# Kernel optimization log

Measured on AMD Instinct MI355X. Metric: run time of the kernel, lower is better.

Reference implementation:

```python
import jax, jax.numpy as jnp
import numpy as np

B, T, F = 8192, 336, 8
H = 20        # lstm_hidden_size
DENSE = 20
OUT = 1
N_LAYERS = 3


def _param(key, shape, scale):
    return jax.random.uniform(key, shape, jnp.float32, -scale, scale)


def setup_inputs() -> dict:
    key = jax.random.key(0)
    ks = jax.random.split(key, 32)
    s = 1.0 / np.sqrt(H)
    inp = {"x": jax.random.normal(ks[0], (B, T, F), jnp.float32)}
    k = 1
    for l in range(N_LAYERS):
        in_size = F if l == 0 else H
        inp[f"W_ih{l}"] = _param(ks[k], (4 * H, in_size), s); k += 1
        inp[f"W_hh{l}"] = _param(ks[k], (4 * H, H), s); k += 1
        inp[f"b_ih{l}"] = _param(ks[k], (4 * H,), s); k += 1
        inp[f"b_hh{l}"] = _param(ks[k], (4 * H,), s); k += 1
    inp["fc1_w"] = _param(ks[k], (DENSE, H), 1.0 / np.sqrt(H)); k += 1
    inp["fc1_b"] = _param(ks[k], (DENSE,), 1.0 / np.sqrt(H)); k += 1
    inp["fc2_w"] = _param(ks[k], (OUT, DENSE), 1.0 / np.sqrt(DENSE)); k += 1
    inp["fc2_b"] = _param(ks[k], (OUT,), 1.0 / np.sqrt(DENSE)); k += 1
    return inp


def lstm_layer(x, W_ih, W_hh, b_ih, b_hh):
    """PyTorch-convention LSTM over [B, T, in]; returns hidden sequence [B, T, H]."""
    b = x.shape[0]
    # Precompute input contribution for all timesteps in one GEMM: [B, T, 4H]
    xg = jnp.einsum('bti,gi->btg', x, W_ih) + b_ih + b_hh
    W_hh_T = W_hh.T  # [H, 4H]

    def step(carry, xt):
        h, c = carry
        gates = xt + h @ W_hh_T                      # [B, 4H], gate order i,f,g,o
        i, f, g, o = jnp.split(gates, 4, axis=-1)
        i = jax.nn.sigmoid(i)
        f = jax.nn.sigmoid(f)
        g = jnp.tanh(g)
        o = jax.nn.sigmoid(o)
        c = f * c + i * g
        h = o * jnp.tanh(c)
        return (h, c), h

    h0 = jnp.zeros((b, W_hh.shape[1]), x.dtype)
    c0 = jnp.zeros_like(h0)
    _, hs = jax.lax.scan(step, (h0, c0), jnp.swapaxes(xg, 0, 1))  # [T, B, H]
    return jnp.swapaxes(hs, 0, 1)


def reference(x, W_ih0, W_hh0, b_ih0, b_hh0, W_ih1, W_hh1, b_ih1, b_hh1,
              W_ih2, W_hh2, b_ih2, b_hh2, fc1_w, fc1_b, fc2_w, fc2_b):
    layers = [(W_ih0, W_hh0, b_ih0, b_hh0),
              (W_ih1, W_hh1, b_ih1, b_hh1),
              (W_ih2, W_hh2, b_ih2, b_hh2)]
    h = x
    for (wi, wh, bi, bh) in layers:
        h = lstm_layer(h, wi, wh, bi, bh)
    h = h[:, -1, :]                         # last timestep, [B, H]
    # dropout layers are identity at inference
    h = jax.nn.relu(h @ fc1_w.T + fc1_b)    # [B, DENSE]
    return h @ fc2_w.T + fc2_b              # [B, OUT]
```

## Files before the change

kernel.cpp:

```cpp
#include <hip/hip_runtime.h>


#define T_LEN 336

typedef _Float16 f16;
typedef _Float16 f16x2 __attribute__((ext_vector_type(2)));
typedef _Float16 f16x4 __attribute__((ext_vector_type(4)));
typedef _Float16 f16x8 __attribute__((ext_vector_type(8)));
typedef float f32x4 __attribute__((ext_vector_type(4)));

#define MFMA(a, b, c) __builtin_amdgcn_mfma_f32_16x16x32_f16((a), (b), (c), 0, 0, 0)

#define SWZ1(n, c) ((c) ^ (((n) & 7) << 3))
#define SWZ0(n, c) ((c) ^ (((n) & 3) << 3))

__device__ __forceinline__ float sigm(float x) {
  return __builtin_amdgcn_rcpf(1.0f + __builtin_amdgcn_exp2f(-1.4426950408889634f * x));
}
__device__ __forceinline__ float tanh_fast(float x) {
  return 2.0f * __builtin_amdgcn_rcpf(1.0f + __builtin_amdgcn_exp2f(-2.8853900817779268f * x)) - 1.0f;
}

#define CELLS4(DI, DF, DG, DO, HV) {                                                        \
  { float i_=sigm((DI)[0]), f_=sigm((DF)[0]), g_=tanh_fast((DG)[0]), o_=sigm((DO)[0]);      \
    c0 = f_*c0 + i_*g_; (HV)[0] = (f16)(o_*tanh_fast(c0)); }                                \
  { float i_=sigm((DI)[1]), f_=sigm((DF)[1]), g_=tanh_fast((DG)[1]), o_=sigm((DO)[1]);      \
    c1 = f_*c1 + i_*g_; (HV)[1] = (f16)(o_*tanh_fast(c1)); }                                \
  { float i_=sigm((DI)[2]), f_=sigm((DF)[2]), g_=tanh_fast((DG)[2]), o_=sigm((DO)[2]);      \
    c2 = f_*c2 + i_*g_; (HV)[2] = (f16)(o_*tanh_fast(c2)); }                                \
  { float i_=sigm((DI)[3]), f_=sigm((DF)[3]), g_=tanh_fast((DG)[3]), o_=sigm((DO)[3]);      \
    c3 = f_*c3 + i_*g_; (HV)[3] = (f16)(o_*tanh_fast(c3)); } }

#define CELL_L(DL, HOUT, GB) {                                                              \
  *(f32x4*)&GB[(q * 16 + n) * 4] = (DL);                                                    \
  float i_ = sigm(GB[n * 4 + q]);                                                           \
  float f_ = sigm(GB[(16 + n) * 4 + q]);                                                    \
  float g_ = tanh_fast(GB[(32 + n) * 4 + q]);                                               \
  float o_ = sigm(GB[(48 + n) * 4 + q]);                                                    \
  cL = f_*cL + i_*g_; HOUT = (f16)(o_*tanh_fast(cL)); }

__global__ __launch_bounds__(192, 2) void lstm3_ws_kernel(
    const float* __restrict__ x,
    const float* __restrict__ Wih0, const float* __restrict__ Whh0,
    const float* __restrict__ bih0, const float* __restrict__ bhh0,
    const float* __restrict__ Wih1, const float* __restrict__ Whh1,
    const float* __restrict__ bih1, const float* __restrict__ bhh1,
    const float* __restrict__ Wih2, const float* __restrict__ Whh2,
    const float* __restrict__ bih2, const float* __restrict__ bhh2,
    const float* __restrict__ fc1w, const float* __restrict__ fc1b,
    const float* __restrict__ fc2w, const float* __restrict__ fc2b,
    float* __restrict__ out)
{
  __shared__ __align__(16) f16 zT0[16 * 32];
  __shared__ __align__(16) f16 zT1[2][16 * 64];
  __shared__ __align__(16) f16 zT2[2][16 * 64];
  __shared__ __align__(16) float gbuf[3][256];
  __shared__ __align__(16) float pbuf[64];

  const int tid  = threadIdx.x;
  const int w    = tid >> 6;
  const int lane = tid & 63;
  const int n = lane & 15;
  const int q = lane >> 4;

  {
    f16x8 zer;
#pragma unroll
    for (int j = 0; j < 8; ++j) zer[j] = (f16)0.f;
    for (int i = tid; i < 64; i += 192)  ((f16x8*)zT0)[i] = zer;
    for (int i = tid; i < 256; i += 192) ((f16x8*)&zT1[0][0])[i] = zer;
    for (int i = tid; i < 256; i += 192) ((f16x8*)&zT2[0][0])[i] = zer;
  }
  __syncthreads();

  auto rowmap = [](int T, int m) { return T < 4 ? T * 20 + m : (m >> 2) * 20 + 16 + (m & 3); };

  f16x8 Fa0{}, Fa1{}, Fa2{}, Fa3{}, Fa4{};
  f16x8 Fb0{}, Fb1{}, Fb2{}, Fb3{}, Fb4{};
  f32x4 Bi{}, Bf{}, Bg{}, Bo{}, BL{};
  float c0 = 0.f, c1 = 0.f, c2 = 0.f, c3 = 0.f, cL = 0.f;

  if (w == 0) {
    auto gA0 = [&](int T) {
      int row = rowmap(T, n);
      f16x8 r;
#pragma unroll
      for (int j = 0; j < 8; ++j) {
        int k = q * 8 + j;
        float v = (k < 8) ? Wih0[row * 8 + k] : (k < 28 ? Whh0[row * 20 + k - 8] : 0.f);
        r[j] = (f16)v;
      }
      return r;
    };
    Fa0 = gA0(0); Fa1 = gA0(1); Fa2 = gA0(2); Fa3 = gA0(3); Fa4 = gA0(4);
    auto gB = [&](int T) {
      f32x4 r;
#pragma unroll
      for (int j = 0; j < 4; ++j) { int row = rowmap(T, q * 4 + j); r[j] = bih0[row] + bhh0[row]; }
      return r;
    };
    Bi = gB(0); Bf = gB(1); Bg = gB(2); Bo = gB(3); BL = gB(4);
  } else {
    const float* Wi = (w == 1) ? Wih1 : Wih2;
    const float* Wh = (w == 1) ? Whh1 : Whh2;
    const float* bi = (w == 1) ? bih1 : bih2;
    const float* bh = (w == 1) ? bhh1 : bhh2;
    auto gA = [&](int T, int c) {
      int row = rowmap(T, n);
      f16x8 r;
#pragma unroll
      for (int j = 0; j < 8; ++j) {
        int k = c * 32 + q * 8 + j;
        float v = (k < 20) ? Wi[row * 20 + k] : (k < 40 ? Wh[row * 20 + k - 20] : 0.f);
        r[j] = (f16)v;
      }
      return r;
    };
    Fa0 = gA(0, 0); Fb0 = gA(0, 1);
    Fa1 = gA(1, 0); Fb1 = gA(1, 1);
    Fa2 = gA(2, 0); Fb2 = gA(2, 1);
    Fa3 = gA(3, 0); Fb3 = gA(3, 1);
    Fa4 = gA(4, 0); Fb4 = gA(4, 1);
    auto gB = [&](int T) {
      f32x4 r;
#pragma unroll
      for (int j = 0; j < 4; ++j) { int row = rowmap(T, q * 4 + j); r[j] = bi[row] + bh[row]; }
      return r;
    };
    Bi = gB(0); Bf = gB(1); Bg = gB(2); Bo = gB(3); BL = gB(4);
  }

  const float* xb = x + (size_t)(blockIdx.x * 16 + n) * (T_LEN * 8) + 4 * q;
  f32x4 xA{}, xB{};
  if (w == 0) {
    xA = *(const f32x4*)(xb);
    xB = *(const f32x4*)(xb + 16);
  }

#pragma unroll 1
  for (int i = 0; i <= T_LEN + 1; ++i) {
    asm volatile("" ::: "memory");
    if (w == 0) {
      if (i < T_LEN) {
        if ((q >> 1) == (i & 1)) {
          f16x4 xh;
          xh[0] = (f16)xA[0]; xh[1] = (f16)xA[1]; xh[2] = (f16)xA[2]; xh[3] = (f16)xA[3];
          *(f16x4*)&zT0[n * 32 + SWZ0(n, 4 * (q & 1))] = xh;
        }
        if (i & 1) {
          xA = xB;
          int pn = (i >> 1) + 2;
          if (pn > (T_LEN / 2 - 1)) pn = T_LEN / 2 - 1;
          xB = *(const f32x4*)(xb + pn * 16);
        }
        f16x8 b0 = *(const f16x8*)&zT0[n * 32 + SWZ0(n, q * 8)];
        f32x4 di = MFMA(Fa0, b0, Bi), df = MFMA(Fa1, b0, Bf),
              dg = MFMA(Fa2, b0, Bg), dn = MFMA(Fa3, b0, Bo),
              dl = MFMA(Fa4, b0, BL);
        f16x4 hv; CELLS4(di, df, dg, dn, hv)
        f16* d1 = &zT1[i & 1][0];
        *(f16x4*)&zT0[n * 32 + SWZ0(n, 8 + q * 4)] = hv;
        *(f16x4*)&d1[n * 64 + SWZ1(n, q * 4)] = hv;
        f16 hl; CELL_L(dl, hl, gbuf[0])
        zT0[n * 32 + SWZ0(n, 24 + q)] = hl;
        d1[n * 64 + SWZ1(n, 16 + q)] = hl;
      }
    } else if (w == 1) {
      if (i >= 1 && i <= T_LEN) {
        const f16* src = &zT1[(i - 1) & 1][0];
        f16x8 ba = *(const f16x8*)&src[n * 64 + SWZ1(n, q * 8)];
        f16x8 bb = *(const f16x8*)&src[n * 64 + SWZ1(n, 32 + q * 8)];
        f32x4 di = MFMA(Fb0, bb, MFMA(Fa0, ba, Bi));
        f32x4 df = MFMA(Fb1, bb, MFMA(Fa1, ba, Bf));
        f32x4 dg = MFMA(Fb2, bb, MFMA(Fa2, ba, Bg));
        f32x4 dn = MFMA(Fb3, bb, MFMA(Fa3, ba, Bo));
        f32x4 dl = MFMA(Fb4, bb, MFMA(Fa4, ba, BL));
        f16x4 hv; CELLS4(di, df, dg, dn, hv)
        f16* d1 = &zT1[i & 1][0];
        f16* d2 = &zT2[i & 1][0];
        *(f16x4*)&d1[n * 64 + SWZ1(n, 20 + q * 4)] = hv;
        *(f16x4*)&d2[n * 64 + SWZ1(n, q * 4)] = hv;
        f16 hl; CELL_L(dl, hl, gbuf[1])
        d1[n * 64 + SWZ1(n, 36 + q)] = hl;
        d2[n * 64 + SWZ1(n, 16 + q)] = hl;
      }
    } else {
      if (i >= 2) {
        const f16* src = &zT2[(i - 1) & 1][0];
        f16x8 ba = *(const f16x8*)&src[n * 64 + SWZ1(n, q * 8)];
        f16x8 bb = *(const f16x8*)&src[n * 64 + SWZ1(n, 32 + q * 8)];
        f32x4 di = MFMA(Fb0, bb, MFMA(Fa0, ba, Bi));
        f32x4 df = MFMA(Fb1, bb, MFMA(Fa1, ba, Bf));
        f32x4 dg = MFMA(Fb2, bb, MFMA(Fa2, ba, Bg));
        f32x4 dn = MFMA(Fb3, bb, MFMA(Fa3, ba, Bo));
        f32x4 dl = MFMA(Fb4, bb, MFMA(Fa4, ba, BL));
        f16x4 hv; CELLS4(di, df, dg, dn, hv)
        f16* d2 = &zT2[i & 1][0];
        *(f16x4*)&d2[n * 64 + SWZ1(n, 20 + q * 4)] = hv;
        f16 hl; CELL_L(dl, hl, gbuf[2])
        d2[n * 64 + SWZ1(n, 36 + q)] = hl;
      }
    }
    asm volatile("s_waitcnt lgkmcnt(0)\n\ts_barrier" ::: "memory");
  }

  if (w == 2) {
    const f16* hb = &zT2[(T_LEN + 1) & 1][0];
    f16x4 hv0 = *(const f16x4*)&hb[n * 64 + SWZ1(n, 20)];
    f16x4 hv1 = *(const f16x4*)&hb[n * 64 + SWZ1(n, 24)];
    f16x4 hv2 = *(const f16x4*)&hb[n * 64 + SWZ1(n, 28)];
    f16x4 hv3 = *(const f16x4*)&hb[n * 64 + SWZ1(n, 32)];
    f16x4 hv4 = *(const f16x4*)&hb[n * 64 + SWZ1(n, 36)];
    float p = 0.f;
#pragma unroll
    for (int i = 0; i < 5; ++i) {
      int d = q * 5 + i;
      const float* wr = fc1w + d * 20;
      float s = fc1b[d]
        + wr[0]  * (float)hv0[0] + wr[1]  * (float)hv0[1] + wr[2]  * (float)hv0[2] + wr[3]  * (float)hv0[3]
        + wr[4]  * (float)hv1[0] + wr[5]  * (float)hv1[1] + wr[6]  * (float)hv1[2] + wr[7]  * (float)hv1[3]
        + wr[8]  * (float)hv2[0] + wr[9]  * (float)hv2[1] + wr[10] * (float)hv2[2] + wr[11] * (float)hv2[3]
        + wr[12] * (float)hv3[0] + wr[13] * (float)hv3[1] + wr[14] * (float)hv3[2] + wr[15] * (float)hv3[3]
        + wr[16] * (float)hv4[0] + wr[17] * (float)hv4[1] + wr[18] * (float)hv4[2] + wr[19] * (float)hv4[3];
      p += fc2w[d] * fmaxf(s, 0.f);
    }
    pbuf[n * 4 + q] = p;
    if (q == 0) {
      f32x4 pv = *(const f32x4*)&pbuf[n * 4];
      out[blockIdx.x * 16 + n] = pv[0] + pv[1] + pv[2] + pv[3] + fc2b[0];
    }
  }
}

extern "C" void kernel_launch(void* const* d_in, const int* in_sizes, int n_in,
                              void* d_out, int out_size, void* d_ws, size_t ws_size,
                              hipStream_t stream) {
  const float* x    = (const float*)d_in[0];
  const float* Wih0 = (const float*)d_in[1];
  const float* Whh0 = (const float*)d_in[2];
  const float* bih0 = (const float*)d_in[3];
  const float* bhh0 = (const float*)d_in[4];
  const float* Wih1 = (const float*)d_in[5];
  const float* Whh1 = (const float*)d_in[6];
  const float* bih1 = (const float*)d_in[7];
  const float* bhh1 = (const float*)d_in[8];
  const float* Wih2 = (const float*)d_in[9];
  const float* Whh2 = (const float*)d_in[10];
  const float* bih2 = (const float*)d_in[11];
  const float* bhh2 = (const float*)d_in[12];
  const float* fc1w = (const float*)d_in[13];
  const float* fc1b = (const float*)d_in[14];
  const float* fc2w = (const float*)d_in[15];
  const float* fc2b = (const float*)d_in[16];
  float* out = (float*)d_out;

  hipLaunchKernelGGL(lstm3_ws_kernel, dim3(8192 / 16), dim3(192), 0, stream,
                     x, Wih0, Whh0, bih0, bhh0,
                     Wih1, Whh1, bih1, bhh1,
                     Wih2, Whh2, bih2, bhh2,
                     fc1w, fc1b, fc2w, fc2b, out);
}
```

Baseline: 463.1 us.

## Process two timesteps per barrier and remap leftover gate rows to avoid LDS transpose

The wavefront-specialized pipeline now runs two LSTM timesteps per loop iteration, so each layer wave does two dependent cell updates between block barriers and the number of barriers is roughly halved. Each layer keeps its own hidden state in a separate ping-pong slot and publishes to the next layer's double-buffered slots. The leftover-gate rows are remapped so each lane holds all four gates of its hidden unit in registers, which removes the per-step gbuf LDS round trip. In exchange it uses more LDS buffers, longer serial chains per barrier interval and more complex index bookkeeping.

Result: faster. 415.2 us (-10.3%).

```diff
diff --git a/kernel.cpp b/kernel.cpp
--- a/kernel.cpp
+++ b/kernel.cpp
@@ -2,9 +2,9 @@
 
 
 #define T_LEN 336
+#define NJ 169
 
 typedef _Float16 f16;
-typedef _Float16 f16x2 __attribute__((ext_vector_type(2)));
 typedef _Float16 f16x4 __attribute__((ext_vector_type(4)));
 typedef _Float16 f16x8 __attribute__((ext_vector_type(8)));
 typedef float f32x4 __attribute__((ext_vector_type(4)));
@@ -12,7 +12,6 @@
 #define MFMA(a, b, c) __builtin_amdgcn_mfma_f32_16x16x32_f16((a), (b), (c), 0, 0, 0)
 
 #define SWZ1(n, c) ((c) ^ (((n) & 7) << 3))
-#define SWZ0(n, c) ((c) ^ (((n) & 3) << 3))
 
 __device__ __forceinline__ float sigm(float x) {
   return __builtin_amdgcn_rcpf(1.0f + __builtin_amdgcn_exp2f(-1.4426950408889634f * x));
@@ -21,7 +20,7 @@
   return 2.0f * __builtin_amdgcn_rcpf(1.0f + __builtin_amdgcn_exp2f(-2.8853900817779268f * x)) - 1.0f;
 }
 
-#define CELLS4(DI, DF, DG, DO, HV) {                                                        \
+#define CELLS5(DI, DF, DG, DO, DL, HV, HL) {                                                \
   { float i_=sigm((DI)[0]), f_=sigm((DF)[0]), g_=tanh_fast((DG)[0]), o_=sigm((DO)[0]);      \
     c0 = f_*c0 + i_*g_; (HV)[0] = (f16)(o_*tanh_fast(c0)); }                                \
   { float i_=sigm((DI)[1]), f_=sigm((DF)[1]), g_=tanh_fast((DG)[1]), o_=sigm((DO)[1]);      \
@@ -29,15 +28,39 @@
   { float i_=sigm((DI)[2]), f_=sigm((DF)[2]), g_=tanh_fast((DG)[2]), o_=sigm((DO)[2]);      \
     c2 = f_*c2 + i_*g_; (HV)[2] = (f16)(o_*tanh_fast(c2)); }                                \
   { float i_=sigm((DI)[3]), f_=sigm((DF)[3]), g_=tanh_fast((DG)[3]), o_=sigm((DO)[3]);      \
-    c3 = f_*c3 + i_*g_; (HV)[3] = (f16)(o_*tanh_fast(c3)); } }
-
-#define CELL_L(DL, HOUT, GB) {                                                              \
-  *(f32x4*)&GB[(q * 16 + n) * 4] = (DL);                                                    \
-  float i_ = sigm(GB[n * 4 + q]);                                                           \
-  float f_ = sigm(GB[(16 + n) * 4 + q]);                                                    \
-  float g_ = tanh_fast(GB[(32 + n) * 4 + q]);                                               \
-  float o_ = sigm(GB[(48 + n) * 4 + q]);                                                    \
-  cL = f_*cL + i_*g_; HOUT = (f16)(o_*tanh_fast(cL)); }
+    c3 = f_*c3 + i_*g_; (HV)[3] = (f16)(o_*tanh_fast(c3)); }                                \
+  { float i_=sigm((DL)[0]), f_=sigm((DL)[1]), g_=tanh_fast((DL)[2]), o_=sigm((DL)[3]);      \
+    cL = f_*cL + i_*g_; (HL) = (f16)(o_*tanh_fast(cL)); } }
+
+#define MIDSTEP(SRC, DSELF, DPUB) {                                                         \
+  const f16* s_ = (SRC);                                                                    \
+  f16x8 ba = *(const f16x8*)&s_[n * 64 + SWZ1(n, q * 8)];                                   \
+  f16x8 bb = *(const f16x8*)&s_[n * 64 + SWZ1(n, 32 + q * 8)];                              \
+  f32x4 di = MFMA(Fb0, bb, MFMA(Fa0, ba, Bi));                                              \
+  f32x4 df = MFMA(Fb1, bb, MFMA(Fa1, ba, Bf));                                              \
+  f32x4 dg = MFMA(Fb2, bb, MFMA(Fa2, ba, Bg));                                              \
+  f32x4 dn = MFMA(Fb3, bb, MFMA(Fa3, ba, Bo));                                              \
+  f32x4 dl = MFMA(Fb4, bb, MFMA(Fa4, ba, BL));                                              \
+  f16x4 hv; f16 hl; CELLS5(di, df, dg, dn, dl, hv, hl)                                      \
+  f16* ds_ = (DSELF);                                                                       \
+  *(f16x4*)&ds_[n * 64 + SWZ1(n, 32 + q * 4)] = hv;                                         \
+  ds_[n * 64 + SWZ1(n, 48 + q)] = hl;                                                       \
+  f16* dp_ = (DPUB);                                                                        \
+  if (dp_) { *(f16x4*)&dp_[n * 64 + SWZ1(n, q * 4)] = hv;                                   \
+             dp_[n * 64 + SWZ1(n, 16 + q)] = hl; } }
+
+#define L0STEP(SRC, DSELF, DPUB) {                                                          \
+  const f16* s_ = (SRC);                                                                    \
+  f16x8 b0 = *(const f16x8*)&s_[n * 64 + SWZ1(n, q * 8)];                                   \
+  f32x4 di = MFMA(Fa0, b0, Bi), df = MFMA(Fa1, b0, Bf), dg = MFMA(Fa2, b0, Bg),             \
+        dn = MFMA(Fa3, b0, Bo), dl = MFMA(Fa4, b0, BL);                                     \
+  f16x4 hv; f16 hl; CELLS5(di, df, dg, dn, dl, hv, hl)                                      \
+  f16* ds_ = (DSELF);                                                                       \
+  *(f16x4*)&ds_[n * 64 + SWZ1(n, 8 + q * 4)] = hv;                                          \
+  ds_[n * 64 + SWZ1(n, 24 + q)] = hl;                                                       \
+  f16* dp_ = (DPUB);                                                                        \
+  *(f16x4*)&dp_[n * 64 + SWZ1(n, q * 4)] = hv;                                              \
+  dp_[n * 64 + SWZ1(n, 16 + q)] = hl; }
 
 __global__ __launch_bounds__(192, 2) void lstm3_ws_kernel(
     const float* __restrict__ x,
@@ -51,10 +74,9 @@
     const float* __restrict__ fc2w, const float* __restrict__ fc2b,
     float* __restrict__ out)
 {
-  __shared__ __align__(16) f16 zT0[16 * 32];
-  __shared__ __align__(16) f16 zT1[2][16 * 64];
-  __shared__ __align__(16) f16 zT2[2][16 * 64];
-  __shared__ __align__(16) float gbuf[3][256];
+  __shared__ __align__(16) f16 zT0[2][16 * 64];
+  __shared__ __align__(16) f16 zT1[2][2][16 * 64];
+  __shared__ __align__(16) f16 zT2[2][2][16 * 64];
   __shared__ __align__(16) float pbuf[64];
 
   const int tid  = threadIdx.x;
@@ -67,13 +89,13 @@
     f16x8 zer;
 #pragma unroll
     for (int j = 0; j < 8; ++j) zer[j] = (f16)0.f;
-    for (int i = tid; i < 64; i += 192)  ((f16x8*)zT0)[i] = zer;
-    for (int i = tid; i < 256; i += 192) ((f16x8*)&zT1[0][0])[i] = zer;
-    for (int i = tid; i < 256; i += 192) ((f16x8*)&zT2[0][0])[i] = zer;
+    for (int i = tid; i < 256; i += 192) ((f16x8*)&zT0[0][0])[i] = zer;
+    for (int i = tid; i < 512; i += 192) ((f16x8*)&zT1[0][0][0])[i] = zer;
+    for (int i = tid; i < 512; i += 192) ((f16x8*)&zT2[0][0][0])[i] = zer;
   }
   __syncthreads();
 
-  auto rowmap = [](int T, int m) { return T < 4 ? T * 20 + m : (m >> 2) * 20 + 16 + (m & 3); };
+  auto rowmap = [](int T, int m) { return T < 4 ? T * 20 + m : (m & 3) * 20 + 16 + (m >> 2); };
 
   f16x8 Fa0{}, Fa1{}, Fa2{}, Fa3{}, Fa4{};
   f16x8 Fb0{}, Fb1{}, Fb2{}, Fb3{}, Fb4{};
@@ -107,12 +129,12 @@
     const float* bh = (w == 1) ? bhh1 : bhh2;
     auto gA = [&](int T, int c) {
       int row = rowmap(T, n);
+      const float* W = c ? Wh : Wi;
       f16x8 r;
 #pragma unroll
       for (int j = 0; j < 8; ++j) {
-        int k = c * 32 + q * 8 + j;
-        float v = (k < 20) ? Wi[row * 20 + k] : (k < 40 ? Wh[row * 20 + k - 20] : 0.f);
-        r[j] = (f16)v;
+        int k = q * 8 + j;
+        r[j] = (f16)((k < 20) ? W[row * 20 + k] : 0.f);
       }
       return r;
     };
@@ -138,79 +160,41 @@
   }
 
 #pragma unroll 1
-  for (int i = 0; i <= T_LEN + 1; ++i) {
+  for (int j = 0; j <= NJ; ++j) {
     asm volatile("" ::: "memory");
+    const int wp = j & 1, rp = wp ^ 1;
     if (w == 0) {
-      if (i < T_LEN) {
-        if ((q >> 1) == (i & 1)) {
-          f16x4 xh;
-          xh[0] = (f16)xA[0]; xh[1] = (f16)xA[1]; xh[2] = (f16)xA[2]; xh[3] = (f16)xA[3];
-          *(f16x4*)&zT0[n * 32 + SWZ0(n, 4 * (q & 1))] = xh;
-        }
-        if (i & 1) {
-          xA = xB;
-          int pn = (i >> 1) + 2;
-          if (pn > (T_LEN / 2 - 1)) pn = T_LEN / 2 - 1;
-          xB = *(const f32x4*)(xb + pn * 16);
-        }
-        f16x8 b0 = *(const f16x8*)&zT0[n * 32 + SWZ0(n, q * 8)];
-        f32x4 di = MFMA(Fa0, b0, Bi), df = MFMA(Fa1, b0, Bf),
-              dg = MFMA(Fa2, b0, Bg), dn = MFMA(Fa3, b0, Bo),
-              dl = MFMA(Fa4, b0, BL);
-        f16x4 hv; CELLS4(di, df, dg, dn, hv)
-        f16* d1 = &zT1[i & 1][0];
-        *(f16x4*)&zT0[n * 32 + SWZ0(n, 8 + q * 4)] = hv;
-        *(f16x4*)&d1[n * 64 + SWZ1(n, q * 4)] = hv;
-        f16 hl; CELL_L(dl, hl, gbuf[0])
-        zT0[n * 32 + SWZ0(n, 24 + q)] = hl;
-        d1[n * 64 + SWZ1(n, 16 + q)] = hl;
+      if (j <= 167) {
+        f16x4 xh;
+        xh[0] = (f16)xA[0]; xh[1] = (f16)xA[1]; xh[2] = (f16)xA[2]; xh[3] = (f16)xA[3];
+        *(f16x4*)&zT0[q >> 1][n * 64 + SWZ1(n, 4 * (q & 1))] = xh;
+        xA = xB;
+        int pn = j + 2; if (pn > 167) pn = 167;
+        xB = *(const f32x4*)(xb + (size_t)pn * 16);
+        L0STEP(&zT0[0][0], &zT0[1][0], &zT1[wp][0][0])
+        L0STEP(&zT0[1][0], &zT0[0][0], &zT1[wp][1][0])
       }
     } else if (w == 1) {
-      if (i >= 1 && i <= T_LEN) {
-        const f16* src = &zT1[(i - 1) & 1][0];
-        f16x8 ba = *(const f16x8*)&src[n * 64 + SWZ1(n, q * 8)];
-        f16x8 bb = *(const f16x8*)&src[n * 64 + SWZ1(n, 32 + q * 8)];
-        f32x4 di = MFMA(Fb0, bb, MFMA(Fa0, ba, Bi));
-        f32x4 df = MFMA(Fb1, bb, MFMA(Fa1, ba, Bf));
-        f32x4 dg = MFMA(Fb2, bb, MFMA(Fa2, ba, Bg));
-        f32x4 dn = MFMA(Fb3, bb, MFMA(Fa3, ba, Bo));
-        f32x4 dl = MFMA(Fb4, bb, MFMA(Fa4, ba, BL));
-        f16x4 hv; CELLS4(di, df, dg, dn, hv)
-        f16* d1 = &zT1[i & 1][0];
-        f16* d2 = &zT2[i & 1][0];
-        *(f16x4*)&d1[n * 64 + SWZ1(n, 20 + q * 4)] = hv;
-        *(f16x4*)&d2[n * 64 + SWZ1(n, q * 4)] = hv;
-        f16 hl; CELL_L(dl, hl, gbuf[1])
-        d1[n * 64 + SWZ1(n, 36 + q)] = hl;
-        d2[n * 64 + SWZ1(n, 16 + q)] = hl;
+      if (j >= 1 && j <= 168) {
+        MIDSTEP(&zT1[rp][0][0], &zT1[rp][1][0], &zT2[wp][0][0])
+        MIDSTEP(&zT1[rp][1][0], &zT1[wp][0][0], &zT2[wp][1][0])
       }
     } else {
-      if (i >= 2) {
-        const f16* src = &zT2[(i - 1) & 1][0];
-        f16x8 ba = *(const f16x8*)&src[n * 64 + SWZ1(n, q * 8)];
-        f16x8 bb = *(const f16x8*)&src[n * 64 + SWZ1(n, 32 + q * 8)];
-        f32x4 di = MFMA(Fb0, bb, MFMA(Fa0, ba, Bi));
-        f32x4 df = MFMA(Fb1, bb, MFMA(Fa1, ba, Bf));
-        f32x4 dg = MFMA(Fb2, bb, MFMA(Fa2, ba, Bg));
-        f32x4 dn = MFMA(Fb3, bb, MFMA(Fa3, ba, Bo));
-        f32x4 dl = MFMA(Fb4, bb, MFMA(Fa4, ba, BL));
-        f16x4 hv; CELLS4(di, df, dg, dn, hv)
-        f16* d2 = &zT2[i & 1][0];
-        *(f16x4*)&d2[n * 64 + SWZ1(n, 20 + q * 4)] = hv;
-        f16 hl; CELL_L(dl, hl, gbuf[2])
-        d2[n * 64 + SWZ1(n, 36 + q)] = hl;
+      if (j >= 2) {
+        MIDSTEP(&zT2[rp][0][0], &zT2[rp][1][0], (f16*)nullptr)
+        MIDSTEP(&zT2[rp][1][0], &zT2[wp][0][0], (f16*)nullptr)
       }
     }
     asm volatile("s_waitcnt lgkmcnt(0)\n\ts_barrier" ::: "memory");
   }
 
   if (w == 2) {
-    const f16* hb = &zT2[(T_LEN + 1) & 1][0];
-    f16x4 hv0 = *(const f16x4*)&hb[n * 64 + SWZ1(n, 20)];
-    f16x4 hv1 = *(const f16x4*)&hb[n * 64 + SWZ1(n, 24)];
-    f16x4 hv2 = *(const f16x4*)&hb[n * 64 + SWZ1(n, 28)];
-    f16x4 hv3 = *(const f16x4*)&hb[n * 64 + SWZ1(n, 32)];
-    f16x4 hv4 = *(const f16x4*)&hb[n * 64 + SWZ1(n, 36)];
+    const f16* hb = &zT2[1][0][0];
+    f16x4 hv0 = *(const f16x4*)&hb[n * 64 + SWZ1(n, 32)];
+    f16x4 hv1 = *(const f16x4*)&hb[n * 64 + SWZ1(n, 36)];
+    f16x4 hv2 = *(const f16x4*)&hb[n * 64 + SWZ1(n, 40)];
+    f16x4 hv3 = *(const f16x4*)&hb[n * 64 + SWZ1(n, 44)];
+    f16x4 hv4 = *(const f16x4*)&hb[n * 64 + SWZ1(n, 48)];
     float p = 0.f;
 #pragma unroll
     for (int i = 0; i < 5; ++i) {
```
